# Performance work log

Hardware: AMD Instinct MI355X
Metric: run time of the kernel (lower is better)

Reference implementation:

```python
import jax, jax.numpy as jnp
import numpy as np

D_MODEL, H, D_FF = 1024, 16, 4096
B, S = 2, 2048
EPS = 1e-05


def layer_norm(x, gamma, beta):
    # Matches torch: mean and UNBIASED std over last dim, scalar gamma/beta,
    # and eps added to std (not variance).
    mean = jnp.mean(x, axis=-1, keepdims=True)
    var = jnp.sum((x - mean) ** 2, axis=-1, keepdims=True) / (x.shape[-1] - 1)
    return gamma * (x - mean) / (jnp.sqrt(var) + EPS) + beta


def setup_inputs() -> dict:
    key = jax.random.key(0)
    ks = jax.random.split(key, 16)
    sd = 1.0 / np.sqrt(D_MODEL)
    sf = 1.0 / np.sqrt(D_FF)
    return {
        "x": jax.random.normal(ks[0], (B, S, D_MODEL), jnp.float32),
        "mask": jnp.ones((1, 1, S, S), jnp.int32),
        "wq": jax.random.uniform(ks[1], (D_MODEL, D_MODEL), jnp.float32, -sd, sd),
        "bq": jax.random.uniform(ks[2], (D_MODEL,), jnp.float32, -sd, sd),
        "wk": jax.random.uniform(ks[3], (D_MODEL, D_MODEL), jnp.float32, -sd, sd),
        "bk": jax.random.uniform(ks[4], (D_MODEL,), jnp.float32, -sd, sd),
        "wv": jax.random.uniform(ks[5], (D_MODEL, D_MODEL), jnp.float32, -sd, sd),
        "bv": jax.random.uniform(ks[6], (D_MODEL,), jnp.float32, -sd, sd),
        "wo": jax.random.uniform(ks[7], (D_MODEL, D_MODEL), jnp.float32, -sd, sd),
        "bo": jax.random.uniform(ks[8], (D_MODEL,), jnp.float32, -sd, sd),
        "w1": jax.random.uniform(ks[9], (D_FF, D_MODEL), jnp.float32, -sd, sd),
        "b1": jax.random.uniform(ks[10], (D_FF,), jnp.float32, -sd, sd),
        "w2": jax.random.uniform(ks[11], (D_MODEL, D_FF), jnp.float32, -sf, sf),
        "b2": jax.random.uniform(ks[12], (D_MODEL,), jnp.float32, -sf, sf),
        "gamma1": jnp.ones((1,), jnp.float32),
        "beta1": jnp.zeros((1,), jnp.float32),
        "gamma2": jnp.ones((1,), jnp.float32),
        "beta2": jnp.zeros((1,), jnp.float32),
    }


def reference(x, mask, wq, bq, wk, bk, wv, bv, wo, bo, w1, b1, w2, b2,
              gamma1, beta1, gamma2, beta2):
    d_k = D_MODEL // H

    # --- residual 1: pre-LN self-attention ---
    xn = layer_norm(x, gamma1, beta1)
    q = (xn @ wq.T + bq).reshape(B, S, H, d_k).transpose(0, 2, 1, 3)
    k = (xn @ wk.T + bk).reshape(B, S, H, d_k).transpose(0, 2, 1, 3)
    v = (xn @ wv.T + bv).reshape(B, S, H, d_k).transpose(0, 2, 1, 3)

    scores = jnp.einsum("bhqd,bhkd->bhqk", q, k) / jnp.sqrt(
        jnp.asarray(d_k, x.dtype))
    scores = jnp.where(mask == 0, jnp.asarray(-1e9, x.dtype), scores)
    attn = jax.nn.softmax(scores, axis=-1)
    ctx = jnp.einsum("bhqk,bhkd->bhqd", attn, v)
    ctx = ctx.transpose(0, 2, 1, 3).reshape(B, S, D_MODEL)
    x = x + (ctx @ wo.T + bo)

    # --- residual 2: pre-LN feed-forward ---
    xn = layer_norm(x, gamma2, beta2)
    h = jax.nn.relu(xn @ w1.T + b1)
    x = x + (h @ w2.T + b2)
    return x
```

## Files before the change

kernel.cpp:

```cpp
#include <hip/hip_runtime.h>


typedef __bf16 bf16_t;
typedef __attribute__((ext_vector_type(8))) __bf16 bf16x8;
typedef __attribute__((ext_vector_type(4))) __bf16 bf16x4;
typedef __attribute__((ext_vector_type(2))) __bf16 bf16x2;
typedef __attribute__((ext_vector_type(4))) float f32x4;
typedef __attribute__((ext_vector_type(16))) float f32x16;
typedef __attribute__((ext_vector_type(2))) unsigned uint32x2;
typedef __attribute__((ext_vector_type(4))) unsigned uint32x4;

#define MB (1024ull * 1024ull)
#define QSCALE 0.18033688011112043f

__device__ __forceinline__ void gload_lds16(const bf16_t* g, bf16_t* l) {
    __builtin_amdgcn_global_load_lds(
        (const __attribute__((address_space(1))) void*)g,
        (__attribute__((address_space(3))) void*)l, 16, 0, 0);
}

__device__ __forceinline__ int bswz(int row) { return ((row >> 1) & 3) << 3; }

__device__ __forceinline__ int swz(int row, int col) {
    return row * 64 + ((((col >> 3) ^ row) & 7) << 3) + (col & 7);
}

__device__ __forceinline__ unsigned cvtpk(float a, float b) {
    bf16x2 v = {(__bf16)a, (__bf16)b};
    return __builtin_bit_cast(unsigned, v);
}

__global__ __launch_bounds__(256) void cvt_all(
    const float* __restrict__ wq, const float* __restrict__ wk,
    const float* __restrict__ wv, const float* __restrict__ wo,
    const float* __restrict__ w1, const float* __restrict__ w2,
    bf16_t* __restrict__ wqkv, bf16_t* __restrict__ wob, bf16_t* __restrict__ w1b,
    bf16_t* __restrict__ w2b) {
    const int b = blockIdx.x, t = threadIdx.x;
    const float* in;
    bf16_t* out;
    int i;
    if (b < 1024) { in = wq; out = wqkv; i = b * 256 + t; }
    else if (b < 2048) { in = wk; out = wqkv + 1048576; i = (b - 1024) * 256 + t; }
    else if (b < 3072) { in = wv; out = wqkv + 2097152; i = (b - 2048) * 256 + t; }
    else if (b < 4096) { in = wo; out = wob; i = (b - 3072) * 256 + t; }
    else if (b < 8192) { in = w1; out = w1b; i = (b - 4096) * 256 + t; }
    else { in = w2; out = w2b; i = (b - 8192) * 256 + t; }
    float4 v = ((const float4*)in)[i];
    bf16x4 o = {(__bf16)v.x, (__bf16)v.y, (__bf16)v.z, (__bf16)v.w};
    ((bf16x4*)out)[i] = o;
}

__global__ __launch_bounds__(256) void ln_kernel(const float* __restrict__ x,
                                                 bf16_t* __restrict__ out,
                                                 const float* __restrict__ gamma,
                                                 const float* __restrict__ beta) {
    const int lane = threadIdx.x & 63;
    const int row = blockIdx.x * 4 + (threadIdx.x >> 6);
    const float* xr = x + (size_t)row * 1024;
    float4 v[4];
    float s = 0.f;
#pragma unroll
    for (int i = 0; i < 4; ++i) {
        v[i] = ((const float4*)xr)[i * 64 + lane];
        s += v[i].x + v[i].y + v[i].z + v[i].w;
    }
#pragma unroll
    for (int o = 32; o; o >>= 1) s += __shfl_xor(s, o);
    float mean = s * (1.f / 1024.f);
    float vs = 0.f;
#pragma unroll
    for (int i = 0; i < 4; ++i) {
        float a = v[i].x - mean, b = v[i].y - mean, c = v[i].z - mean, d = v[i].w - mean;
        vs += a * a + b * b + c * c + d * d;
    }
#pragma unroll
    for (int o = 32; o; o >>= 1) vs += __shfl_xor(vs, o);
    float inv = 1.f / (sqrtf(vs * (1.f / 1023.f)) + 1e-5f);
    float g = gamma[0] * inv, bb = beta[0];
    bf16_t* orow = out + (size_t)row * 1024;
#pragma unroll
    for (int i = 0; i < 4; ++i) {
        bf16x4 ov = {(__bf16)((v[i].x - mean) * g + bb), (__bf16)((v[i].y - mean) * g + bb),
                     (__bf16)((v[i].z - mean) * g + bb), (__bf16)((v[i].w - mean) * g + bb)};
        *(bf16x4*)(orow + (i * 64 + lane) * 4) = ov;
    }
}

template <int KERN>
__global__ __launch_bounds__(512, 2) void gemm256(
    const bf16_t* __restrict__ A, const bf16_t* __restrict__ Bw, int K,
    const float* __restrict__ bias0, const float* __restrict__ bias1,
    const float* __restrict__ bias2, void* __restrict__ o0, void* __restrict__ o1,
    void* __restrict__ o2) {
    __shared__ bf16_t L[4 * 16384];
    const int t = threadIdx.x, lane = t & 63, w = t >> 6;
    const int wm = w >> 2, wn = w & 3;
    const int l15 = lane & 15, l4 = lane >> 4;
    const int bm = blockIdx.x, bn = blockIdx.y;
    const int NT = K >> 5;
    const bf16_t* Ab = A + (size_t)bm * 256 * K;
    const bf16_t* Bb = Bw + (size_t)bn * 256 * K;
    const int srow = t >> 2, pcol = (t & 3) * 8;
    f32x4 acc[8][4] = {};

    auto stageA = [&](int tt) {
        bf16_t* s = L + (tt & 3) * 16384;
        const int kb = tt * 32;
#pragma unroll
        for (int i = 0; i < 2; ++i) {
            int row = i * 128 + srow;
            int lcol = pcol ^ bswz(row);
            gload_lds16(Ab + (size_t)row * K + kb + lcol, s + i * 4096 + t * 8);
        }
    };
    auto stageB = [&](int tt) {
        bf16_t* s = L + (tt & 3) * 16384 + 8192;
        const int kb = tt * 32;
#pragma unroll
        for (int i = 0; i < 2; ++i) {
            int row = i * 128 + srow;
            int lcol = pcol ^ bswz(row);
            gload_lds16(Bb + (size_t)row * K + kb + lcol, s + i * 4096 + t * 8);
        }
    };

    stageA(0); stageB(0); stageA(1); stageB(1); stageA(2); stageB(2);
    asm volatile("s_waitcnt vmcnt(8)" ::: "memory");
    __builtin_amdgcn_s_barrier();

    for (int tt = 0; tt < NT; ++tt) {
        bf16_t* s = L + (tt & 3) * 16384;
        bf16_t* sB = s + 8192;
        bf16x8 af[4], bfr[4];
#pragma unroll
        for (int m = 0; m < 4; ++m) {
            int row = wm * 128 + m * 16 + l15;
            af[m] = *(const bf16x8*)(s + row * 32 + ((l4 * 8) ^ bswz(row)));
        }
#pragma unroll
        for (int n = 0; n < 4; ++n) {
            int row = wn * 64 + n * 16 + l15;
            bfr[n] = *(const bf16x8*)(sB + row * 32 + ((l4 * 8) ^ bswz(row)));
        }
        if (tt + 3 < NT) stageA(tt + 3);
        __builtin_amdgcn_s_barrier();
        __builtin_amdgcn_s_setprio(1);
#pragma unroll
        for (int m = 0; m < 4; ++m)
#pragma unroll
            for (int n = 0; n < 4; ++n)
                acc[m][n] = __builtin_amdgcn_mfma_f32_16x16x32_bf16(af[m], bfr[n], acc[m][n],
                                                                   0, 0, 0);
        __builtin_amdgcn_s_setprio(0);
        __builtin_amdgcn_s_barrier();
#pragma unroll
        for (int m = 0; m < 4; ++m) {
            int row = wm * 128 + 64 + m * 16 + l15;
            af[m] = *(const bf16x8*)(s + row * 32 + ((l4 * 8) ^ bswz(row)));
        }
        if (tt + 3 < NT) stageB(tt + 3);
        __builtin_amdgcn_s_barrier();
        __builtin_amdgcn_s_setprio(1);
#pragma unroll
        for (int m = 0; m < 4; ++m)
#pragma unroll
            for (int n = 0; n < 4; ++n)
                acc[4 + m][n] = __builtin_amdgcn_mfma_f32_16x16x32_bf16(af[m], bfr[n],
                                                                       acc[4 + m][n], 0, 0, 0);
        __builtin_amdgcn_s_setprio(0);
        if (tt + 3 < NT)
            asm volatile("s_waitcnt vmcnt(8)" ::: "memory");
        else if (tt + 2 < NT)
            asm volatile("s_waitcnt vmcnt(4)" ::: "memory");
        else
            asm volatile("s_waitcnt vmcnt(0)" ::: "memory");
        __builtin_amdgcn_s_barrier();
    }

    if (KERN == 1) {
        const int colb = bn * 256 + wn * 64;
        float bb[4];
#pragma unroll
        for (int n = 0; n < 4; ++n) bb[n] = bias0[colb + n * 16 + l15];
#pragma unroll
        for (int m = 0; m < 8; ++m) {
            const int row0 = bm * 256 + wm * 128 + m * 16 + (l4 << 2);
#pragma unroll
            for (int n = 0; n < 4; ++n)
#pragma unroll
                for (int j = 0; j < 4; ++j) {
                    float v = acc[m][n][j] + bb[n];
                    ((bf16_t*)o0)[(size_t)(row0 + j) * 4096 + colb + n * 16 + l15] =
                        (bf16_t)(v > 0.f ? v : 0.f);
                }
        }
        return;
    }
    if (bn < 8) {
        const bool isq = bn < 4;
        const float* bias = isq ? bias0 : bias1;
        const int head = (bn & 3) * 4 + wn;
        const int b = (bm * 256) >> 11;
        const int srow0 = (bm * 256 + wm * 128) & 2047;
        bf16_t* dst = (bf16_t*)(isq ? o0 : o1) + ((size_t)(b * 16 + head) << 17);
        float bb[4];
#pragma unroll
        for (int n = 0; n < 4; ++n) bb[n] = bias[head * 64 + n * 16 + l15];
#pragma unroll
        for (int m = 0; m < 8; ++m)
#pragma unroll
            for (int n = 0; n < 4; ++n)
#pragma unroll
                for (int j = 0; j < 4; ++j) {
                    int srw = srow0 + m * 16 + (l4 << 2) + j;
                    float v = acc[m][n][j] + bb[n];
                    if (isq) v *= QSCALE;
                    dst[((size_t)srw << 6) + n * 16 + l15] = (bf16_t)v;
                }
    } else {
        const int head = (bn - 8) * 4 + wn;
        const int b = (bm * 256) >> 11;
        const int sbase = (bm * 256 + wm * 128) & 2047;
        bf16_t* P = L + w * 8192;
        float bb[4];
#pragma unroll
        for (int n = 0; n < 4; ++n) bb[n] = bias2[head * 64 + n * 16 + l15];
#pragma unroll
        for (int m = 0; m < 8; ++m)
#pragma unroll
            for (int n = 0; n < 4; ++n) {
                int d = n * 16 + l15;
                int sl = m * 16 + (l4 << 2);
                bf16x4 pk = {(__bf16)(acc[m][n][0] + bb[n]), (__bf16)(acc[m][n][1] + bb[n]),
                             (__bf16)(acc[m][n][2] + bb[n]), (__bf16)(acc[m][n][3] + bb[n])};
                *(bf16x4*)(P + d * 128 + (sl ^ ((d & 7) << 3))) = pk;
            }
#pragma unroll
        for (int p = 0; p < 16; ++p) {
            int id = p * 64 + lane;
            int d = id >> 4, c8 = (id & 15) * 8;
            bf16x8 vv = *(const bf16x8*)(P + d * 128 + (c8 ^ ((d & 7) << 3)));
            *(bf16x8*)((bf16_t*)o2 + (((size_t)(b * 16 + head) * 64 + d) << 11) + sbase + c8) =
                vv;
        }
    }
}

template <int SPLIT>
__global__ __launch_bounds__(256, 2) void gemm128sq(
    const bf16_t* __restrict__ A, const bf16_t* __restrict__ Bw, int stride, int Ks,
    const float* __restrict__ bias, const float* __restrict__ resid,
    void* __restrict__ o0, void* __restrict__ o1) {
    __shared__ bf16_t L[4 * 8192];
    const int t = threadIdx.x, lane = t & 63, w = t >> 6;
    const int wr = w >> 1, wc = w & 1;
    const int l15 = lane & 15, l4 = lane >> 4;
    const int bm = blockIdx.x, bn = blockIdx.y;
    const int NT = Ks >> 5;
    const size_t kofs = SPLIT ? (size_t)blockIdx.z * Ks : 0;
    const bf16_t* Ab = A + (size_t)bm * 128 * stride + kofs;
    const bf16_t* Bb = Bw + (size_t)bn * 128 * stride + kofs;
    const int srow = t >> 2, pcol = (t & 3) * 8;
    f32x4 acc[4][4] = {};

    auto STAGE = [&](int tt) {
        bf16_t* s = L + (tt & 3) * 8192;
        const int kb = tt * 32;
#pragma unroll
        for (int i = 0; i < 2; ++i) {
            int row = i * 64 + srow;
            int lcol = pcol ^ bswz(row);
            gload_lds16(Ab + (size_t)row * stride + kb + lcol, s + i * 2048 + t * 8);
            gload_lds16(Bb + (size_t)row * stride + kb + lcol, s + 4096 + i * 2048 + t * 8);
        }
    };

    STAGE(0); STAGE(1); STAGE(2);
    asm volatile("s_waitcnt vmcnt(8)" ::: "memory");
    __builtin_amdgcn_s_barrier();

    for (int tt = 0; tt < NT; ++tt) {
        bf16_t* s = L + (tt & 3) * 8192;
        bf16x8 af[4], bfr[4];
#pragma unroll
        for (int m = 0; m < 4; ++m) {
            int row = wr * 64 + m * 16 + l15;
            af[m] = *(const bf16x8*)(s + row * 32 + ((l4 * 8) ^ bswz(row)));
        }
#pragma unroll
        for (int n = 0; n < 4; ++n) {
            int row = wc * 64 + n * 16 + l15;
            bfr[n] = *(const bf16x8*)(s + 4096 + row * 32 + ((l4 * 8) ^ bswz(row)));
        }
        if (tt + 3 < NT) STAGE(tt + 3);
        __builtin_amdgcn_s_barrier();
        __builtin_amdgcn_s_setprio(1);
#pragma unroll
        for (int m = 0; m < 4; ++m)
#pragma unroll
            for (int n = 0; n < 4; ++n)
                acc[m][n] = __builtin_amdgcn_mfma_f32_16x16x32_bf16(af[m], bfr[n], acc[m][n],
                                                                   0, 0, 0);
        __builtin_amdgcn_s_setprio(0);
        if (tt + 3 < NT)
            asm volatile("s_waitcnt vmcnt(8)" ::: "memory");
        else if (tt + 2 < NT)
            asm volatile("s_waitcnt vmcnt(4)" ::: "memory");
        else
            asm volatile("s_waitcnt vmcnt(0)" ::: "memory");
        __builtin_amdgcn_s_barrier();
    }

#pragma unroll
    for (int m = 0; m < 4; ++m) {
        const int row0 = bm * 128 + wr * 64 + m * 16 + (l4 << 2);
#pragma unroll
        for (int n = 0; n < 4; ++n) {
            const int col = bn * 128 + wc * 64 + n * 16 + l15;
#pragma unroll
            for (int j = 0; j < 4; ++j) {
                const int row = row0 + j;
                if (SPLIT == 0) {
                    ((float*)o0)[(size_t)row * 1024 + col] =
                        resid[(size_t)row * 1024 + col] + acc[m][n][j] + bias[col];
                } else {
                    bf16_t* po = (bf16_t*)(blockIdx.z ? o1 : o0);
                    po[(size_t)row * 1024 + col] = (bf16_t)acc[m][n][j];
                }
            }
        }
    }
}

__global__ __launch_bounds__(256) void ffn2_combine(
    const bf16_t* __restrict__ p0, const bf16_t* __restrict__ p1,
    const float* __restrict__ resid, const float* __restrict__ bias,
    float* __restrict__ out) {
    int i = blockIdx.x * 256 + threadIdx.x;
    float4 r = ((const float4*)resid)[i];
    bf16x4 a = ((const bf16x4*)p0)[i];
    bf16x4 b = ((const bf16x4*)p1)[i];
    float4 bs = ((const float4*)bias)[i & 255];
    float4 o;
    o.x = r.x + (float)a.x + (float)b.x + bs.x;
    o.y = r.y + (float)a.y + (float)b.y + bs.y;
    o.z = r.z + (float)a.z + (float)b.z + bs.z;
    o.w = r.w + (float)a.w + (float)b.w + bs.w;
    ((float4*)out)[i] = o;
}

__global__ __launch_bounds__(256, 2) void attn_split(const bf16_t* __restrict__ q,
                                                     const bf16_t* __restrict__ k,
                                                     const bf16_t* __restrict__ vt,
                                                     bf16_t* __restrict__ opart,
                                                     float2* __restrict__ ml) {
    __shared__ bf16_t Kl[64 * 64];
    __shared__ bf16_t Vl[64 * 64];
    const int t = threadIdx.x, lane = t & 63, w = t >> 6;
    const int bid = blockIdx.x;
    const int xcd = bid & 7, j = bid >> 3;
    const int bh = xcd + ((j >> 5) << 3);
    const int qx = (j & 31) >> 1;
    const int half = j & 1;
    const int sbase = half << 10;
    const bf16_t* qg = q + (size_t)bh * 2048 * 64;
    const bf16_t* kg = k + (size_t)bh * 2048 * 64;
    const bf16_t* vg = vt + (size_t)bh * 64 * 2048;
    const int r = t >> 3, c8 = (t & 7) * 8;
    const int l31 = lane & 31, h = lane >> 5;
    const int rowl = w * 32 + l31;
    const int qrow = qx * 128 + rowl;

    bf16x8 qf[4];
#pragma unroll
    for (int kd = 0; kd < 4; ++kd)
        qf[kd] = *(const bf16x8*)(qg + (size_t)qrow * 64 + kd * 16 + h * 8);

    f32x16 o0 = {}, o1 = {};
    float mi = -1e30f, li = 0.f;

    {
        bf16x8 k0 = *(const bf16x8*)(kg + (size_t)(sbase + r) * 64 + c8);
        bf16x8 k1 = *(const bf16x8*)(kg + (size_t)(sbase + r + 32) * 64 + c8);
        bf16x8 v0 = *(const bf16x8*)(vg + (size_t)r * 2048 + sbase + c8);
        bf16x8 v1 = *(const bf16x8*)(vg + (size_t)(r + 32) * 2048 + sbase + c8);
        *(bf16x8*)(Kl + swz(r, c8)) = k0;
        *(bf16x8*)(Kl + swz(r + 32, c8)) = k1;
        *(bf16x8*)(Vl + swz(r, c8)) = v0;
        *(bf16x8*)(Vl + swz(r + 32, c8)) = v1;
    }

    for (int kt = 0; kt < 1024; kt += 64) {
        __syncthreads();
        bf16x8 k0, k1, v0, v1;
        const bool more = (kt + 64) < 1024;
        if (more) {
            k0 = *(const bf16x8*)(kg + (size_t)(sbase + kt + 64 + r) * 64 + c8);
            k1 = *(const bf16x8*)(kg + (size_t)(sbase + kt + 64 + r + 32) * 64 + c8);
            v0 = *(const bf16x8*)(vg + (size_t)r * 2048 + sbase + kt + 64 + c8);
            v1 = *(const bf16x8*)(vg + (size_t)(r + 32) * 2048 + sbase + kt + 64 + c8);
        }
        f32x16 sT0 = {}, sT1 = {};
        __builtin_amdgcn_s_setprio(1);
#pragma unroll
        for (int kd = 0; kd < 4; ++kd) {
            bf16x8 ka0 = *(const bf16x8*)(Kl + swz(l31, kd * 16 + h * 8));
            bf16x8 ka1 = *(const bf16x8*)(Kl + swz(32 + l31, kd * 16 + h * 8));
            sT0 = __builtin_amdgcn_mfma_f32_32x32x16_bf16(ka0, qf[kd], sT0, 0, 0, 0);
            sT1 = __builtin_amdgcn_mfma_f32_32x32x16_bf16(ka1, qf[kd], sT1, 0, 0, 0);
        }
        __builtin_amdgcn_s_setprio(0);
        float mx = fmaxf(sT0[0], sT0[1]);
#pragma unroll
        for (int i = 2; i < 16; ++i) mx = fmaxf(mx, sT0[i]);
#pragma unroll
        for (int i = 0; i < 16; ++i) mx = fmaxf(mx, sT1[i]);
        mx = fmaxf(mx, __shfl_xor(mx, 32));
        if (!__all(mx <= mi + 8.f)) {
            float mn = fmaxf(mi, mx);
            float al = __builtin_amdgcn_exp2f(mi - mn);
            mi = mn;
            li *= al;
            o0 *= al;
            o1 *= al;
        }
        f32x16 e0, e1;
        float rs = 0.f;
#pragma unroll
        for (int i = 0; i < 16; ++i) {
            e0[i] = __builtin_amdgcn_exp2f(sT0[i] - mi);
            rs += e0[i];
        }
#pragma unroll
        for (int i = 0; i < 16; ++i) {
            e1[i] = __builtin_amdgcn_exp2f(sT1[i] - mi);
            rs += e1[i];
        }
        rs += __shfl_xor(rs, 32);
        li += rs;
        bf16x8 pa[4];
#pragma unroll
        for (int kd = 0; kd < 4; ++kd) {
            const f32x16& e = (kd < 2) ? e0 : e1;
            const int R0l = 8 * (kd & 1);
            const int R0h = R0l + 4;
            unsigned U0 = cvtpk(e[R0l + 0], e[R0l + 1]);
            unsigned V0 = cvtpk(e[R0l + 2], e[R0l + 3]);
            unsigned U1 = cvtpk(e[R0h + 0], e[R0h + 1]);
            unsigned V1 = cvtpk(e[R0h + 2], e[R0h + 3]);
            uint32x2 ru = __builtin_amdgcn_permlane32_swap(U0, U1, false, false);
            uint32x2 rv = __builtin_amdgcn_permlane32_swap(V0, V1, false, false);
            uint32x4 pw = {ru.x, rv.x, ru.y, rv.y};
            pa[kd] = __builtin_bit_cast(bf16x8, pw);
        }
        __builtin_amdgcn_s_setprio(1);
#pragma unroll
        for (int kd = 0; kd < 4; ++kd) {
            bf16x8 va0 = *(const bf16x8*)(Vl + swz(l31, kd * 16 + h * 8));
            bf16x8 va1 = *(const bf16x8*)(Vl + swz(32 + l31, kd * 16 + h * 8));
            o0 = __builtin_amdgcn_mfma_f32_32x32x16_bf16(va0, pa[kd], o0, 0, 0, 0);
            o1 = __builtin_amdgcn_mfma_f32_32x32x16_bf16(va1, pa[kd], o1, 0, 0, 0);
        }
        __builtin_amdgcn_s_setprio(0);
        __syncthreads();
        if (more) {
            *(bf16x8*)(Kl + swz(r, c8)) = k0;
            *(bf16x8*)(Kl + swz(r + 32, c8)) = k1;
            *(bf16x8*)(Vl + swz(r, c8)) = v0;
            *(bf16x8*)(Vl + swz(r + 32, c8)) = v1;
        }
    }
    const int combo = bh * 16 + qx;
    bf16_t* op = opart + ((size_t)half << 22) + (size_t)combo * 8192 + (size_t)rowl * 64;
#pragma unroll
    for (int g = 0; g < 4; ++g) {
        bf16x4 ov0 = {(__bf16)o0[4 * g + 0], (__bf16)o0[4 * g + 1], (__bf16)o0[4 * g + 2],
                      (__bf16)o0[4 * g + 3]};
        *(bf16x4*)(op + 8 * g + 4 * h) = ov0;
        bf16x4 ov1 = {(__bf16)o1[4 * g + 0], (__bf16)o1[4 * g + 1], (__bf16)o1[4 * g + 2],
                      (__bf16)o1[4 * g + 3]};
        *(bf16x4*)(op + 32 + 8 * g + 4 * h) = ov1;
    }
    if (h == 0) ml[((size_t)half * 512 + combo) * 128 + rowl] = make_float2(mi, li);
}

__global__ __launch_bounds__(256) void attn_merge(const bf16_t* __restrict__ opart,
                                                  const float2* __restrict__ ml,
                                                  bf16_t* __restrict__ ctx) {
    const int combo = blockIdx.x >> 2;
    const int row = (blockIdx.x & 3) * 32 + (threadIdx.x >> 3);
    const int d8 = (threadIdx.x & 7) * 8;
    float2 a = ml[(size_t)combo * 128 + row];
    float2 b = ml[(size_t)(512 + combo) * 128 + row];
    float m = fmaxf(a.x, b.x);
    float ea = __builtin_amdgcn_exp2f(a.x - m), eb = __builtin_amdgcn_exp2f(b.x - m);
    float inv = 1.f / (a.y * ea + b.y * eb);
    float ia = ea * inv, ib = eb * inv;
    size_t po = (size_t)combo * 8192 + (size_t)row * 64 + d8;
    bf16x8 u = *(const bf16x8*)(opart + po);
    bf16x8 v = *(const bf16x8*)(opart + (1ull << 22) + po);
    bf16x8 o;
#pragma unroll
    for (int jj = 0; jj < 8; ++jj) o[jj] = (__bf16)((float)u[jj] * ia + (float)v[jj] * ib);
    const int bh = combo >> 4, qx = combo & 15;
    const int rg = qx * 128 + row;
    *(bf16x8*)(ctx + ((size_t)(bh >> 4) * 2048 + rg) * 1024 + (bh & 15) * 64 + d8) = o;
}

extern "C" void kernel_launch(void* const* d_in, const int* in_sizes, int n_in,
                              void* d_out, int out_size, void* d_ws, size_t ws_size,
                              hipStream_t stream) {
    const float* x = (const float*)d_in[0];
    const float* wq = (const float*)d_in[2];
    const float* bq = (const float*)d_in[3];
    const float* wk = (const float*)d_in[4];
    const float* bk = (const float*)d_in[5];
    const float* wv = (const float*)d_in[6];
    const float* bv = (const float*)d_in[7];
    const float* wo = (const float*)d_in[8];
    const float* bo = (const float*)d_in[9];
    const float* w1 = (const float*)d_in[10];
    const float* b1 = (const float*)d_in[11];
    const float* w2 = (const float*)d_in[12];
    const float* b2 = (const float*)d_in[13];
    const float* gamma1 = (const float*)d_in[14];
    const float* beta1 = (const float*)d_in[15];
    const float* gamma2 = (const float*)d_in[16];
    const float* beta2 = (const float*)d_in[17];

    char* ws = (char*)d_ws;
    bf16_t* wqkv = (bf16_t*)(ws + 0);
    bf16_t* wob = (bf16_t*)(ws + 6 * MB);
    bf16_t* w1b = (bf16_t*)(ws + 8 * MB);
    bf16_t* w2b = (bf16_t*)(ws + 16 * MB);
    bf16_t* xnb = (bf16_t*)(ws + 24 * MB);
    bf16_t* qb = (bf16_t*)(ws + 32 * MB);
    bf16_t* kb = (bf16_t*)(ws + 40 * MB);
    bf16_t* vtb = (bf16_t*)(ws + 48 * MB);
    bf16_t* ctxb = (bf16_t*)(ws + 56 * MB);
    float* x1 = (float*)(ws + 64 * MB);
    bf16_t* hb = (bf16_t*)(ws + 32 * MB);
    bf16_t* opart = (bf16_t*)(ws + 64 * MB);
    float2* mlbuf = (float2*)(ws + 0);
    bf16_t* p0 = (bf16_t*)(ws + 0);
    bf16_t* p1 = (bf16_t*)(ws + 24 * MB);

    cvt_all<<<12288, 256, 0, stream>>>(wq, wk, wv, wo, w1, w2, wqkv, wob, w1b, w2b);

    ln_kernel<<<1024, 256, 0, stream>>>(x, xnb, gamma1, beta1);
    gemm256<0><<<dim3(16, 12), 512, 0, stream>>>(xnb, wqkv, 1024, bq, bk, bv, qb, kb, vtb);
    attn_split<<<1024, 256, 0, stream>>>(qb, kb, vtb, opart, mlbuf);
    attn_merge<<<2048, 256, 0, stream>>>(opart, mlbuf, ctxb);
    gemm128sq<0><<<dim3(32, 8), 256, 0, stream>>>(ctxb, wob, 1024, 1024, bo, x, x1, nullptr);
    ln_kernel<<<1024, 256, 0, stream>>>(x1, xnb, gamma2, beta2);
    gemm256<1><<<dim3(16, 16), 512, 0, stream>>>(xnb, w1b, 1024, b1, nullptr, nullptr, hb,
                                                 nullptr, nullptr);
    gemm128sq<1><<<dim3(32, 8, 2), 256, 0, stream>>>(hb, w2b, 4096, 2048, nullptr, nullptr,
                                                     p0, p1);
    ffn2_combine<<<4096, 256, 0, stream>>>(p0, p1, x1, b2, (float*)d_out);
}
```

Before: 221.3 us.

## Double-buffer attention K/V tiles with direct global-to-LDS loads

The attention split kernel now stages K and V tiles straight into a double-buffered LDS ring using global_load_lds, waiting with explicit vmcnt counts instead of going through registers and storing to LDS after a second barrier. It also turns the row max and row sum into tree reductions and raises the launch-bounds occupancy hint from 2 to 4 blocks. The goal is to overlap the next tile's loads with the current tile's MFMA work and shorten serial dependency chains. In exchange it doubles LDS per block and tightens register limits, which could cause spills, and it relies on hand-written waitcnt and barrier ordering being correct.

```diff
diff --git a/kernel.cpp b/kernel.cpp
--- a/kernel.cpp
+++ b/kernel.cpp
@@ -350,13 +350,13 @@
     ((float4*)out)[i] = o;
 }
 
-__global__ __launch_bounds__(256, 2) void attn_split(const bf16_t* __restrict__ q,
+__global__ __launch_bounds__(256, 4) void attn_split(const bf16_t* __restrict__ q,
                                                      const bf16_t* __restrict__ k,
                                                      const bf16_t* __restrict__ vt,
                                                      bf16_t* __restrict__ opart,
                                                      float2* __restrict__ ml) {
-    __shared__ bf16_t Kl[64 * 64];
-    __shared__ bf16_t Vl[64 * 64];
+    __shared__ bf16_t Kl[2][64 * 64];
+    __shared__ bf16_t Vl[2][64 * 64];
     const int t = threadIdx.x, lane = t & 63, w = t >> 6;
     const int bid = blockIdx.x;
     const int xcd = bid & 7, j = bid >> 3;
@@ -367,10 +367,11 @@
     const bf16_t* qg = q + (size_t)bh * 2048 * 64;
     const bf16_t* kg = k + (size_t)bh * 2048 * 64;
     const bf16_t* vg = vt + (size_t)bh * 64 * 2048;
-    const int r = t >> 3, c8 = (t & 7) * 8;
     const int l31 = lane & 31, h = lane >> 5;
     const int rowl = w * 32 + l31;
     const int qrow = qx * 128 + rowl;
+    const int prow = t >> 3, p = t & 7;
+    const int sc = ((p ^ prow) & 7) * 8;
 
     bf16x8 qf[4];
 #pragma unroll
@@ -380,43 +381,46 @@
     f32x16 o0 = {}, o1 = {};
     float mi = -1e30f, li = 0.f;
 
-    {
-        bf16x8 k0 = *(const bf16x8*)(kg + (size_t)(sbase + r) * 64 + c8);
-        bf16x8 k1 = *(const bf16x8*)(kg + (size_t)(sbase + r + 32) * 64 + c8);
-        bf16x8 v0 = *(const bf16x8*)(vg + (size_t)r * 2048 + sbase + c8);
-        bf16x8 v1 = *(const bf16x8*)(vg + (size_t)(r + 32) * 2048 + sbase + c8);
-        *(bf16x8*)(Kl + swz(r, c8)) = k0;
-        *(bf16x8*)(Kl + swz(r + 32, c8)) = k1;
-        *(bf16x8*)(Vl + swz(r, c8)) = v0;
-        *(bf16x8*)(Vl + swz(r + 32, c8)) = v1;
-    }
-
-    for (int kt = 0; kt < 1024; kt += 64) {
-        __syncthreads();
-        bf16x8 k0, k1, v0, v1;
-        const bool more = (kt + 64) < 1024;
-        if (more) {
-            k0 = *(const bf16x8*)(kg + (size_t)(sbase + kt + 64 + r) * 64 + c8);
-            k1 = *(const bf16x8*)(kg + (size_t)(sbase + kt + 64 + r + 32) * 64 + c8);
-            v0 = *(const bf16x8*)(vg + (size_t)r * 2048 + sbase + kt + 64 + c8);
-            v1 = *(const bf16x8*)(vg + (size_t)(r + 32) * 2048 + sbase + kt + 64 + c8);
-        }
+    auto STAGE = [&](int tt) {
+        bf16_t* kd_ = Kl[tt & 1];
+        bf16_t* vd_ = Vl[tt & 1];
+        const int kb = sbase + tt * 64;
+        gload_lds16(kg + (size_t)(kb + prow) * 64 + sc, kd_ + t * 8);
+        gload_lds16(kg + (size_t)(kb + prow + 32) * 64 + sc, kd_ + 2048 + t * 8);
+        gload_lds16(vg + (size_t)prow * 2048 + kb + sc, vd_ + t * 8);
+        gload_lds16(vg + (size_t)(prow + 32) * 2048 + kb + sc, vd_ + 2048 + t * 8);
+    };
+
+    STAGE(0);
+    const int NT = 16;
+    for (int tt = 0; tt < NT; ++tt) {
+        if (tt + 1 < NT) {
+            STAGE(tt + 1);
+            asm volatile("s_waitcnt vmcnt(4)" ::: "memory");
+        } else {
+            asm volatile("s_waitcnt vmcnt(0)" ::: "memory");
+        }
+        __builtin_amdgcn_s_barrier();
+        const bf16_t* Kb = Kl[tt & 1];
+        const bf16_t* Vb = Vl[tt & 1];
         f32x16 sT0 = {}, sT1 = {};
         __builtin_amdgcn_s_setprio(1);
 #pragma unroll
         for (int kd = 0; kd < 4; ++kd) {
-            bf16x8 ka0 = *(const bf16x8*)(Kl + swz(l31, kd * 16 + h * 8));
-            bf16x8 ka1 = *(const bf16x8*)(Kl + swz(32 + l31, kd * 16 + h * 8));
+            bf16x8 ka0 = *(const bf16x8*)(Kb + swz(l31, kd * 16 + h * 8));
+            bf16x8 ka1 = *(const bf16x8*)(Kb + swz(32 + l31, kd * 16 + h * 8));
             sT0 = __builtin_amdgcn_mfma_f32_32x32x16_bf16(ka0, qf[kd], sT0, 0, 0, 0);
             sT1 = __builtin_amdgcn_mfma_f32_32x32x16_bf16(ka1, qf[kd], sT1, 0, 0, 0);
         }
         __builtin_amdgcn_s_setprio(0);
-        float mx = fmaxf(sT0[0], sT0[1]);
-#pragma unroll
-        for (int i = 2; i < 16; ++i) mx = fmaxf(mx, sT0[i]);
-#pragma unroll
-        for (int i = 0; i < 16; ++i) mx = fmaxf(mx, sT1[i]);
-        mx = fmaxf(mx, __shfl_xor(mx, 32));
+        float pm[16];
+#pragma unroll
+        for (int i = 0; i < 16; ++i) pm[i] = fmaxf(sT0[i], sT1[i]);
+#pragma unroll
+        for (int st = 8; st; st >>= 1)
+#pragma unroll
+            for (int i = 0; i < st; ++i) pm[i] = fmaxf(pm[i], pm[i + st]);
+        float mx = fmaxf(pm[0], __shfl_xor(pm[0], 32));
         if (!__all(mx <= mi + 8.f)) {
             float mn = fmaxf(mi, mx);
             float al = __builtin_amdgcn_exp2f(mi - mn);
@@ -426,19 +430,18 @@
             o1 *= al;
         }
         f32x16 e0, e1;
-        float rs = 0.f;
-#pragma unroll
-        for (int i = 0; i < 16; ++i) {
-            e0[i] = __builtin_amdgcn_exp2f(sT0[i] - mi);
-            rs += e0[i];
-        }
-#pragma unroll
-        for (int i = 0; i < 16; ++i) {
-            e1[i] = __builtin_amdgcn_exp2f(sT1[i] - mi);
-            rs += e1[i];
-        }
-        rs += __shfl_xor(rs, 32);
-        li += rs;
+#pragma unroll
+        for (int i = 0; i < 16; ++i) e0[i] = __builtin_amdgcn_exp2f(sT0[i] - mi);
+#pragma unroll
+        for (int i = 0; i < 16; ++i) e1[i] = __builtin_amdgcn_exp2f(sT1[i] - mi);
+        float ps[16];
+#pragma unroll
+        for (int i = 0; i < 16; ++i) ps[i] = e0[i] + e1[i];
+#pragma unroll
+        for (int st = 8; st; st >>= 1)
+#pragma unroll
+            for (int i = 0; i < st; ++i) ps[i] += ps[i + st];
+        li += ps[0] + __shfl_xor(ps[0], 32);
         bf16x8 pa[4];
 #pragma unroll
         for (int kd = 0; kd < 4; ++kd) {
@@ -457,19 +460,13 @@
         __builtin_amdgcn_s_setprio(1);
 #pragma unroll
         for (int kd = 0; kd < 4; ++kd) {
-            bf16x8 va0 = *(const bf16x8*)(Vl + swz(l31, kd * 16 + h * 8));
-            bf16x8 va1 = *(const bf16x8*)(Vl + swz(32 + l31, kd * 16 + h * 8));
+            bf16x8 va0 = *(const bf16x8*)(Vb + swz(l31, kd * 16 + h * 8));
+            bf16x8 va1 = *(const bf16x8*)(Vb + swz(32 + l31, kd * 16 + h * 8));
             o0 = __builtin_amdgcn_mfma_f32_32x32x16_bf16(va0, pa[kd], o0, 0, 0, 0);
             o1 = __builtin_amdgcn_mfma_f32_32x32x16_bf16(va1, pa[kd], o1, 0, 0, 0);
         }
         __builtin_amdgcn_s_setprio(0);
-        __syncthreads();
-        if (more) {
-            *(bf16x8*)(Kl + swz(r, c8)) = k0;
-            *(bf16x8*)(Kl + swz(r + 32, c8)) = k1;
-            *(bf16x8*)(Vl + swz(r, c8)) = v0;
-            *(bf16x8*)(Vl + swz(r + 32, c8)) = v1;
-        }
+        __builtin_amdgcn_s_barrier();
     }
     const int combo = bh * 16 + qx;
     bf16_t* op = opart + ((size_t)half << 22) + (size_t)combo * 8192 + (size_t)rowl * 64;
```

Result: no change. 219.4 us (-0.9%).
